# Performance work log

Hardware: AMD Instinct MI355X
Metric: run time of the kernel (lower is better)

Reference implementation:

```python
import jax, jax.numpy as jnp
import numpy as np

NTYPES = 2
MAXNEI = 128      # maxNeighborNum
M2 = 16
NPER = 256        # atoms per type
B = 4
EMB = [25, 50, 100]
FIT_IN = M2 * EMB[-1]  # 1600
FH = 240


def setup_inputs() -> dict:
    key = jax.random.key(0)
    ks = jax.random.split(key, 16)
    s = 0.1
    inp = {
        "Ri": jax.random.normal(ks[0], (B, NTYPES * NPER, NTYPES * MAXNEI, 4), jnp.float32),
        "emb_W0": jax.random.normal(ks[1], (4, 1, EMB[0]), jnp.float32) * s,
        "emb_b0": jax.random.normal(ks[2], (4, EMB[0]), jnp.float32) * s,
        "emb_W1": jax.random.normal(ks[3], (4, EMB[0], EMB[1]), jnp.float32) * s,
        "emb_b1": jax.random.normal(ks[4], (4, EMB[1]), jnp.float32) * s,
        "emb_W2": jax.random.normal(ks[5], (4, EMB[1], EMB[2]), jnp.float32) * s,
        "emb_b2": jax.random.normal(ks[6], (4, EMB[2]), jnp.float32) * s,
        "fit_W0": jax.random.normal(ks[7], (2, FIT_IN, FH), jnp.float32) * 0.02,
        "fit_b0": jax.random.normal(ks[8], (2, FH), jnp.float32) * s,
        "fit_W1": jax.random.normal(ks[9], (2, FH, FH), jnp.float32) * 0.05,
        "fit_b1": jax.random.normal(ks[10], (2, FH), jnp.float32) * s,
        "fit_W2": jax.random.normal(ks[11], (2, FH, FH), jnp.float32) * 0.05,
        "fit_b2": jax.random.normal(ks[12], (2, FH), jnp.float32) * s,
        "fit_W3": jax.random.normal(ks[13], (2, FH, 1), jnp.float32) * 0.05,
        "fit_b3": jax.random.normal(ks[14], (2, 1), jnp.float32),
    }
    return inp


def _emb(s, W0, b0, W1, b1, W2, b2):
    # DeepMD-style embedding MLP with doubling resnet skips (1->25->50->100)
    h0 = jnp.tanh(s @ W0 + b0)
    h1 = jnp.tanh(h0 @ W1 + b1) + jnp.concatenate([h0, h0], axis=-1)
    h2 = jnp.tanh(h1 @ W2 + b2) + jnp.concatenate([h1, h1], axis=-1)
    return h2


def _fit(d, W0, b0, W1, b1, W2, b2, W3, b3):
    h = jnp.tanh(d @ W0 + b0)
    h = jnp.tanh(h @ W1 + b1) + h   # resnet skip (equal dims)
    h = jnp.tanh(h @ W2 + b2) + h
    return h @ W3 + b3              # [B, N, 1]


def reference(Ri, emb_W0, emb_b0, emb_W1, emb_b1, emb_W2, emb_b2,
              fit_W0, fit_b0, fit_W1, fit_b1, fit_W2, fit_b2, fit_W3, fit_b3):
    type_nums = NTYPES
    Ei_blocks = []
    for i in range(NTYPES):                      # center-atom type
        Ri_i = Ri[:, i * NPER:(i + 1) * NPER]    # [B, NPER, NTYPES*M, 4]
        xyz = None
        for j in range(NTYPES):                  # neighbor type
            blk = Ri_i[:, :, j * MAXNEI:(j + 1) * MAXNEI, :]  # [B,N,M,4]
            S = blk[..., 0:1]                                  # [B,N,M,1]
            e = i * NTYPES + j
            G = _emb(S, emb_W0[e], emb_b0[e], emb_W1[e], emb_b1[e],
                     emb_W2[e], emb_b2[e])                     # [B,N,M,100]
            tmp = jnp.einsum('bnmc,bnmg->bncg', blk, G)        # [B,N,4,100]
            xyz = tmp if xyz is None else xyz + tmp
        xyz = xyz / (MAXNEI * type_nums)
        xyz_b = xyz[..., :M2]                                  # [B,N,4,16]
        DR = jnp.einsum('bncg,bnch->bngh', xyz, xyz_b)         # [B,N,100,16]
        DR = DR.reshape(B, NPER, FIT_IN)
        Ei_i = _fit(DR, fit_W0[i], fit_b0[i], fit_W1[i], fit_b1[i],
                    fit_W2[i], fit_b2[i], fit_W3[i], fit_b3[i])  # [B,N,1]
        Ei_blocks.append(Ei_i)
    Ei = jnp.concatenate(Ei_blocks, axis=1)     # [B, natoms_sum, 1]
    return Ei[..., 0]                            # per-atom energies [B, natoms_sum]
```

## Files before the change

### kernel.cpp

```cpp
#include <hip/hip_runtime.h>
#include <hip/hip_bf16.h>

#define FH 240
#define FIT_IN 1600
#define NK 2048
#define TLO -16.0f
#define TINVH 64.0f

typedef _Float16 h8 __attribute__((ext_vector_type(8)));
typedef float f4v __attribute__((ext_vector_type(4)));

__device__ __forceinline__ float fast_tanh(float x) {
    float e2 = __builtin_amdgcn_exp2f(x * 2.8853900817779268f);
    return 1.0f - 2.0f * __builtin_amdgcn_rcpf(e2 + 1.0f);
}

#define FMA_ROW(r, s) \
    acc[r][0] += (s) * b0.x; acc[r][1] += (s) * b0.y; \
    acc[r][2] += (s) * b0.z; acc[r][3] += (s) * b0.w; \
    acc[r][4] += (s) * b1.x; acc[r][5] += (s) * b1.y; \
    acc[r][6] += (s) * b1.z; acc[r][7] += (s) * b1.w;

#define TOFF_W0   0
#define TOFF_B0   28
#define TOFF_B1   56
#define TOFF_B2   108
#define TOFF_W1   208
#define TOFF_W2   1508
#define TOFF_H0T  6708
#define TOFF_H1T  10008
#define TSMEM     16608

__global__ __launch_bounds__(256) void k_prep(
    const float* __restrict__ eW0, const float* __restrict__ eB0,
    const float* __restrict__ eW1, const float* __restrict__ eB1,
    const float* __restrict__ eW2, const float* __restrict__ eB2,
    float* __restrict__ T,
    const float* __restrict__ fW0, const float* __restrict__ fW1,
    const float* __restrict__ fW2,
    _Float16* __restrict__ W0T, _Float16* __restrict__ W1T,
    _Float16* __restrict__ W2T)
{
    __shared__ float sm[TSMEM];
    const int t = threadIdx.x;

    if (blockIdx.x >= 64) {
        const int bid0 = blockIdx.x - 64;
        const int total = 768000 + 115200 + 115200;
        for (int idx = bid0 * 256 + t; idx < total; idx += 448 * 256) {
            if (idx < 768000) {
                const int tp = idx / 384000, r = idx - tp * 384000;
                const int n = r / 1600, k = r - n * 1600;
                W0T[idx] = (_Float16)fW0[tp * 384000 + k * 240 + n];
            } else if (idx < 883200) {
                const int j = idx - 768000;
                const int tp = j / 57600, r = j - tp * 57600;
                const int n = r / 240, k = r - n * 240;
                W1T[j] = (_Float16)fW1[tp * 57600 + k * 240 + n];
            } else {
                const int j = idx - 883200;
                const int tp = j / 57600, r = j - tp * 57600;
                const int n = r / 240, k = r - n * 240;
                W2T[j] = (_Float16)fW2[tp * 57600 + k * 240 + n];
            }
        }
        return;
    }

    const int w    = t >> 6;
    const int lane = t & 63;
    const int mi   = lane & 7;
    const int gi   = lane >> 3;
    const int mrow = w * 32 + mi * 4;

    const int e  = blockIdx.x >> 4;
    const int k0 = (blockIdx.x & 15) * 128;

    for (int idx = t; idx < 1250; idx += 256) {
        int k = idx / 50, g = idx - k * 50;
        sm[TOFF_W1 + k * 52 + g] = eW1[e * 1250 + idx];
    }
    for (int idx = t; idx < 5000; idx += 256) {
        int k = idx / 100, r = idx - k * 100;
        int half = r / 50, g = r - half * 50;
        sm[TOFF_W2 + k * 104 + half * 52 + g] = eW2[e * 5000 + idx];
    }
    if (t < 25)       { sm[TOFF_W0 + t] = eW0[e * 25 + t]; sm[TOFF_B0 + t] = eB0[e * 25 + t]; }
    else if (t < 75)  { sm[TOFF_B1 + (t - 25)] = eB1[e * 50 + (t - 25)]; }
    else if (t < 175) { sm[TOFF_B2 + (t - 75)] = eB2[e * 100 + (t - 75)]; }
    __syncthreads();

    if (t < 128) {
        const float S = TLO + (float)(k0 + t) * (1.0f / TINVH);
        #pragma unroll
        for (int k = 0; k < 25; ++k)
            sm[TOFF_H0T + k * 132 + t] = fast_tanh(S * sm[TOFF_W0 + k] + sm[TOFF_B0 + k]);
    }
    __syncthreads();

    {
        float acc[4][8];
        #pragma unroll
        for (int r = 0; r < 4; ++r)
            #pragma unroll
            for (int c = 0; c < 8; ++c) acc[r][c] = 0.f;

        #pragma unroll 5
        for (int k = 0; k < 25; ++k) {
            const float4 av = *(const float4*)&sm[TOFF_H0T + k * 132 + mrow];
            const float4 b0 = *(const float4*)&sm[TOFF_W1 + k * 52 + gi * 8];
            const float4 b1 = *(const float4*)&sm[TOFF_W1 + k * 52 + gi * 8 + 4];
            FMA_ROW(0, av.x) FMA_ROW(1, av.y) FMA_ROW(2, av.z) FMA_ROW(3, av.w)
        }
        #pragma unroll
        for (int c = 0; c < 8; ++c) {
            const int g = gi * 8 + c;
            if (g < 50) {
                const int gm = (g < 25) ? g : g - 25;
                const float4 h0r = *(const float4*)&sm[TOFF_H0T + gm * 132 + mrow];
                const float bias = sm[TOFF_B1 + g];
                float4 o;
                o.x = fast_tanh(acc[0][c] + bias) + h0r.x;
                o.y = fast_tanh(acc[1][c] + bias) + h0r.y;
                o.z = fast_tanh(acc[2][c] + bias) + h0r.z;
                o.w = fast_tanh(acc[3][c] + bias) + h0r.w;
                *(float4*)&sm[TOFF_H1T + g * 132 + mrow] = o;
            }
        }
    }
    __syncthreads();

    for (int half = 0; half < 2; ++half) {
        float acc[4][8];
        #pragma unroll
        for (int r = 0; r < 4; ++r)
            #pragma unroll
            for (int c = 0; c < 8; ++c) acc[r][c] = 0.f;

        #pragma unroll 5
        for (int k = 0; k < 50; ++k) {
            const float4 av = *(const float4*)&sm[TOFF_H1T + k * 132 + mrow];
            const float4 b0 = *(const float4*)&sm[TOFF_W2 + k * 104 + half * 52 + gi * 8];
            const float4 b1 = *(const float4*)&sm[TOFF_W2 + k * 104 + half * 52 + gi * 8 + 4];
            FMA_ROW(0, av.x) FMA_ROW(1, av.y) FMA_ROW(2, av.z) FMA_ROW(3, av.w)
        }
        #pragma unroll
        for (int c = 0; c < 8; ++c) {
            const int g = gi * 8 + c;
            if (g < 50) {
                const float4 h1r = *(const float4*)&sm[TOFF_H1T + g * 132 + mrow];
                const float bias = sm[TOFF_B2 + half * 50 + g];
                float* out = T + ((size_t)e * NK + k0 + mrow) * 100 + half * 50 + g;
                out[0]   = fast_tanh(acc[0][c] + bias) + h1r.x;
                out[100] = fast_tanh(acc[1][c] + bias) + h1r.y;
                out[200] = fast_tanh(acc[2][c] + bias) + h1r.z;
                out[300] = fast_tanh(acc[3][c] + bias) + h1r.w;
            }
        }
    }
}

__global__ __launch_bounds__(256) void k_xyz(
    const float* __restrict__ Ri, const float* __restrict__ T,
    _Float16* __restrict__ DRh)
{
    __shared__ float4 sR[256];
    __shared__ float  sF[256];
    __shared__ int    sI[256];
    __shared__ float  sXYZ[400];

    const int t   = threadIdx.x;
    const int blk = blockIdx.x;
    const int b   = blk >> 9;
    const int i   = (blk >> 8) & 1;
    const int n   = blk & 255;

    for (int idx = t; idx < 400; idx += 256) sXYZ[idx] = 0.f;

    {
        const int jj = t >> 7, m = t & 127;
        const size_t row = ((size_t)(b * 512 + i * 256 + n)) * 256 + jj * 128 + m;
        const float4 r = *(const float4*)(Ri + row * 4);
        sR[t] = r;
        float u = (r.x - TLO) * TINVH;
        int ii = (int)u;
        ii = (ii < 0) ? 0 : ((ii > NK - 2) ? NK - 2 : ii);
        sI[t] = ii;
        sF[t] = u - (float)ii;
    }
    __syncthreads();

    const int jj = t >> 7;
    const int g  = t & 127;
    if (g < 100) {
        const float* Te = T + ((size_t)(i * 2 + jj)) * NK * 100 + g;
        float a0 = 0.f, a1 = 0.f, a2 = 0.f, a3 = 0.f;
        #pragma unroll 4
        for (int m = 0; m < 128; ++m) {
            const int s = jj * 128 + m;
            const float4 R = sR[s];
            const float  f = sF[s];
            const float* p = Te + (size_t)sI[s] * 100;
            const float v0 = p[0], v1 = p[100];
            const float G = v0 + f * (v1 - v0);
            a0 += R.x * G; a1 += R.y * G; a2 += R.z * G; a3 += R.w * G;
        }
        atomicAdd(&sXYZ[g],       a0);
        atomicAdd(&sXYZ[100 + g], a1);
        atomicAdd(&sXYZ[200 + g], a2);
        atomicAdd(&sXYZ[300 + g], a3);
    }
    __syncthreads();

    const float inv = 1.0f / 65536.0f;
    _Float16* dr = DRh + (((size_t)i * 4 + b) * 256 + n) * FIT_IN;
    for (int q = t; q < 400; q += 256) {
        const int gg = q >> 2, h0 = (q & 3) * 4;
        ushort4 pk;
        _Float16* ph = (_Float16*)&pk;
        #pragma unroll
        for (int r = 0; r < 4; ++r) {
            const int h = h0 + r;
            const float v = (sXYZ[gg] * sXYZ[h] + sXYZ[100 + gg] * sXYZ[100 + h]
                           + sXYZ[200 + gg] * sXYZ[200 + h] + sXYZ[300 + gg] * sXYZ[300 + h]) * inv;
            ph[r] = (_Float16)v;
        }
        *(ushort4*)(dr + gg * 16 + h0) = pk;
    }
}

__global__ __launch_bounds__(512) void k_fit(
    const _Float16* __restrict__ DRh,
    const _Float16* __restrict__ W0T, const _Float16* __restrict__ W1T,
    const _Float16* __restrict__ W2T,
    const float* __restrict__ fb0, const float* __restrict__ fb1,
    const float* __restrict__ fb2, const float* __restrict__ fW3,
    const float* __restrict__ fb3, float* __restrict__ out)
{
    __shared__ _Float16 sB[2][240 * 40];
    __shared__ _Float16 sA0[2][16 * 40];
    __shared__ _Float16 sA[16 * 264];
    __shared__ float    hRes[2][8 * 240];

    const int t    = threadIdx.x;
    const int w    = t >> 6;
    const int lane = t & 63;
    const int ln   = lane & 15;
    const int quad = lane >> 4;
    const int r0   = blockIdx.x * 8;
    const int tp   = r0 >> 10;
    const int nf0  = w * 2;
    const int nfr  = (w < 7) ? 2 : 1;

    for (int q = t; q < 16 * 264; q += 512) sA[q] = (_Float16)0.f;
    for (int q = t; q < 2 * 16 * 40; q += 512) ((_Float16*)sA0)[q] = (_Float16)0.f;

    const _Float16* Ab = DRh + (size_t)r0 * FIT_IN;
    const _Float16* Wb = W0T + (size_t)tp * 240 * FIT_IN;

    f4v acc[2];
    acc[0] = (f4v)0.f; acc[1] = (f4v)0.f;
    {
        uint2 pB[4]; uint2 pA;
        {
            const int k0 = 0;
            #pragma unroll
            for (int j = 0; j < 4; ++j) {
                const int q = t + j * 512;
                if (q < 1920) {
                    const int n = q >> 3, kq = (q & 7) * 4;
                    pB[j] = *(const uint2*)(Wb + (size_t)n * FIT_IN + k0 + kq);
                }
            }
            if (t < 64) {
                const int m = t >> 3, kq = (t & 7) * 4;
                pA = *(const uint2*)(Ab + (size_t)m * FIT_IN + k0 + kq);
            }
        }
        for (int step = 0; step < 50; ++step) {
            const int buf = step & 1;
            #pragma unroll
            for (int j = 0; j < 4; ++j) {
                const int q = t + j * 512;
                if (q < 1920) {
                    const int n = q >> 3, kq = (q & 7) * 4;
                    *(uint2*)&sB[buf][n * 40 + kq] = pB[j];
                }
            }
            if (t < 64) {
                const int m = t >> 3, kq = (t & 7) * 4;
                *(uint2*)&sA0[buf][m * 40 + kq] = pA;
            }
            __syncthreads();
            if (step < 49) {
                const int k0 = (step + 1) * 32;
                #pragma unroll
                for (int j = 0; j < 4; ++j) {
                    const int q = t + j * 512;
                    if (q < 1920) {
                        const int n = q >> 3, kq = (q & 7) * 4;
                        pB[j] = *(const uint2*)(Wb + (size_t)n * FIT_IN + k0 + kq);
                    }
                }
                if (t < 64) {
                    const int m = t >> 3, kq = (t & 7) * 4;
                    pA = *(const uint2*)(Ab + (size_t)m * FIT_IN + k0 + kq);
                }
            }
            const h8 afr = *(const h8*)&sA0[buf][ln * 40 + quad * 8];
            #pragma unroll
            for (int nf = 0; nf < 2; ++nf) {
                if (nf < nfr) {
                    const h8 bfr = *(const h8*)&sB[buf][((nf0 + nf) * 16 + ln) * 40 + quad * 8];
                    acc[nf] = __builtin_amdgcn_mfma_f32_16x16x32_f16(afr, bfr, acc[nf], 0, 0, 0);
                }
            }
        }
    }
    __syncthreads();
    {
        const float* B0 = fb0 + tp * FH;
        #pragma unroll
        for (int nf = 0; nf < 2; ++nf) {
            if (nf < nfr && quad < 2) {
                const int col = (nf0 + nf) * 16 + ln;
                const float bias = B0[col];
                #pragma unroll
                for (int r = 0; r < 4; ++r) {
                    const int m = quad * 4 + r;
                    const float v = fast_tanh(acc[nf][r] + bias);
                    hRes[0][m * 240 + col] = v;
                    sA[m * 264 + col] = (_Float16)v;
                }
            }
        }
    }
    __syncthreads();

    for (int layer = 0; layer < 2; ++layer) {
        const _Float16* Wt = (layer == 0 ? W1T : W2T) + (size_t)tp * FH * FH;
        const float* Bias  = (layer == 0 ? fb1 : fb2) + tp * FH;
        const float* res   = hRes[layer];
        float* outb        = hRes[layer ^ 1];

        f4v a2[2];
        a2[0] = (f4v)0.f; a2[1] = (f4v)0.f;
        uint2 pW[4];
        #pragma unroll
        for (int j = 0; j < 4; ++j) {
            const int q = t + j * 512;
            if (q < 1920) {
                const int n = q >> 3, kq = (q & 7) * 4;
                pW[j] = (kq < FH) ? *(const uint2*)(Wt + (size_t)n * FH + kq)
                                  : make_uint2(0u, 0u);
            }
        }
        for (int step = 0; step < 8; ++step) {
            const int buf = step & 1;
            #pragma unroll
            for (int j = 0; j < 4; ++j) {
                const int q = t + j * 512;
                if (q < 1920) {
                    const int n = q >> 3, kq = (q & 7) * 4;
                    *(uint2*)&sB[buf][n * 40 + kq] = pW[j];
                }
            }
            __syncthreads();
            if (step < 7) {
                const int k0 = (step + 1) * 32;
                #pragma unroll
                for (int j = 0; j < 4; ++j) {
                    const int q = t + j * 512;
                    if (q < 1920) {
                        const int n = q >> 3, kq = (q & 7) * 4;
                        const int k = k0 + kq;
                        pW[j] = (k < FH) ? *(const uint2*)(Wt + (size_t)n * FH + k)
                                         : make_uint2(0u, 0u);
                    }
                }
            }
            const int k0 = step * 32;
            const h8 afr = *(const h8*)&sA[ln * 264 + k0 + quad * 8];
            #pragma unroll
            for (int nf = 0; nf < 2; ++nf) {
                if (nf < nfr) {
                    const h8 bfr = *(const h8*)&sB[buf][((nf0 + nf) * 16 + ln) * 40 + quad * 8];
                    a2[nf] = __builtin_amdgcn_mfma_f32_16x16x32_f16(afr, bfr, a2[nf], 0, 0, 0);
                }
            }
        }
        __syncthreads();
        #pragma unroll
        for (int nf = 0; nf < 2; ++nf) {
            if (nf < nfr && quad < 2) {
                const int col = (nf0 + nf) * 16 + ln;
                const float bias = Bias[col];
                #pragma unroll
                for (int r = 0; r < 4; ++r) {
                    const int m = quad * 4 + r;
                    const float v = fast_tanh(a2[nf][r] + bias) + res[m * 240 + col];
                    outb[m * 240 + col] = v;
                    if (layer == 0) sA[m * 264 + col] = (_Float16)v;
                }
            }
        }
        __syncthreads();
    }

    {
        const float* h2 = hRes[0];
        const float* wv = fW3 + tp * FH;
        const int m = w;
        float s = 0.f;
        #pragma unroll
        for (int k = lane; k < FH; k += 64) s += h2[m * 240 + k] * wv[k];
        #pragma unroll
        for (int off = 32; off > 0; off >>= 1) s += __shfl_down(s, off);
        if (lane == 0) {
            const int gr = r0 + m;
            const int rem = gr & 1023;
            const int b = rem >> 8, n = rem & 255;
            out[b * 512 + tp * 256 + n] = s + fb3[tp];
        }
    }
}

extern "C" void kernel_launch(void* const* d_in, const int* in_sizes, int n_in,
                              void* d_out, int out_size, void* d_ws, size_t ws_size,
                              hipStream_t stream)
{
    const float* Ri  = (const float*)d_in[0];
    const float* eW0 = (const float*)d_in[1];
    const float* eB0 = (const float*)d_in[2];
    const float* eW1 = (const float*)d_in[3];
    const float* eB1 = (const float*)d_in[4];
    const float* eW2 = (const float*)d_in[5];
    const float* eB2 = (const float*)d_in[6];
    const float* fW0 = (const float*)d_in[7];
    const float* fb0 = (const float*)d_in[8];
    const float* fW1 = (const float*)d_in[9];
    const float* fb1 = (const float*)d_in[10];
    const float* fW2 = (const float*)d_in[11];
    const float* fb2 = (const float*)d_in[12];
    const float* fW3 = (const float*)d_in[13];
    const float* fb3 = (const float*)d_in[14];

    char* p = (char*)d_ws;
    float* T   = (float*)p;                 p += (size_t)4 * NK * 100 * 4;
    _Float16* DRh = (_Float16*)p;           p += (size_t)2048 * FIT_IN * 2;
    _Float16* W0T = (_Float16*)p;           p += (size_t)768000 * 2;
    _Float16* W1T = (_Float16*)p;           p += (size_t)115200 * 2;
    _Float16* W2T = (_Float16*)p;           p += (size_t)115200 * 2;

    k_prep<<<dim3(512), dim3(256), 0, stream>>>(eW0, eB0, eW1, eB1, eW2, eB2, T,
                                                fW0, fW1, fW2, W0T, W1T, W2T);
    k_xyz<<<dim3(2048), dim3(256), 0, stream>>>(Ri, T, DRh);
    k_fit<<<dim3(256), dim3(512), 0, stream>>>(DRh, W0T, W1T, W2T,
                                               fb0, fb1, fb2, fW3, fb3,
                                               (float*)d_out);
}
```

Baseline: 174.2 us.

## Load fit-MLP MFMA fragments directly from global memory with register prefetch

The fitting kernel's GEMMs no longer stage the weight and DR tiles through double-buffered shared memory. Each lane now loads its MFMA A/B fragments straight from global memory, with a two-step register prefetch for the first layer and a one-step prefetch for the hidden layers. This removes the LDS stores and the per-step __syncthreads across the 50-step K loop and the 8-step hidden loops. In exchange it relies on the caches for weight reuse across warps and blocks, and the hidden layers drop the k<240 guard. That means they read past each 240-wide row, and past the end of the last weight row, multiplying the overrun by zero-padded activations.

```diff
diff --git a/kernel.cpp b/kernel.cpp
--- a/kernel.cpp
+++ b/kernel.cpp
@@ -237,8 +237,6 @@
     const float* __restrict__ fb2, const float* __restrict__ fW3,
     const float* __restrict__ fb3, float* __restrict__ out)
 {
-    __shared__ _Float16 sB[2][240 * 40];
-    __shared__ _Float16 sA0[2][16 * 40];
     __shared__ _Float16 sA[16 * 264];
     __shared__ float    hRes[2][8 * 240];
 
@@ -253,71 +251,38 @@
     const int nfr  = (w < 7) ? 2 : 1;
 
     for (int q = t; q < 16 * 264; q += 512) sA[q] = (_Float16)0.f;
-    for (int q = t; q < 2 * 16 * 40; q += 512) ((_Float16*)sA0)[q] = (_Float16)0.f;
-
-    const _Float16* Ab = DRh + (size_t)r0 * FIT_IN;
-    const _Float16* Wb = W0T + (size_t)tp * 240 * FIT_IN;
 
     f4v acc[2];
     acc[0] = (f4v)0.f; acc[1] = (f4v)0.f;
     {
-        uint2 pB[4]; uint2 pA;
-        {
-            const int k0 = 0;
-            #pragma unroll
-            for (int j = 0; j < 4; ++j) {
-                const int q = t + j * 512;
-                if (q < 1920) {
-                    const int n = q >> 3, kq = (q & 7) * 4;
-                    pB[j] = *(const uint2*)(Wb + (size_t)n * FIT_IN + k0 + kq);
-                }
-            }
-            if (t < 64) {
-                const int m = t >> 3, kq = (t & 7) * 4;
-                pA = *(const uint2*)(Ab + (size_t)m * FIT_IN + k0 + kq);
-            }
-        }
-        for (int step = 0; step < 50; ++step) {
-            const int buf = step & 1;
-            #pragma unroll
-            for (int j = 0; j < 4; ++j) {
-                const int q = t + j * 512;
-                if (q < 1920) {
-                    const int n = q >> 3, kq = (q & 7) * 4;
-                    *(uint2*)&sB[buf][n * 40 + kq] = pB[j];
-                }
-            }
-            if (t < 64) {
-                const int m = t >> 3, kq = (t & 7) * 4;
-                *(uint2*)&sA0[buf][m * 40 + kq] = pA;
-            }
-            __syncthreads();
-            if (step < 49) {
-                const int k0 = (step + 1) * 32;
-                #pragma unroll
-                for (int j = 0; j < 4; ++j) {
-                    const int q = t + j * 512;
-                    if (q < 1920) {
-                        const int n = q >> 3, kq = (q & 7) * 4;
-                        pB[j] = *(const uint2*)(Wb + (size_t)n * FIT_IN + k0 + kq);
-                    }
-                }
-                if (t < 64) {
-                    const int m = t >> 3, kq = (t & 7) * 4;
-                    pA = *(const uint2*)(Ab + (size_t)m * FIT_IN + k0 + kq);
-                }
-            }
-            const h8 afr = *(const h8*)&sA0[buf][ln * 40 + quad * 8];
-            #pragma unroll
-            for (int nf = 0; nf < 2; ++nf) {
-                if (nf < nfr) {
-                    const h8 bfr = *(const h8*)&sB[buf][((nf0 + nf) * 16 + ln) * 40 + quad * 8];
-                    acc[nf] = __builtin_amdgcn_mfma_f32_16x16x32_f16(afr, bfr, acc[nf], 0, 0, 0);
-                }
-            }
-        }
-    }
-    __syncthreads();
+        const _Float16* Arow = DRh + (size_t)(r0 + (ln & 7)) * FIT_IN;
+        const _Float16* W0b  = W0T + (size_t)tp * 240 * FIT_IN;
+        const _Float16* Bp0  = W0b + (size_t)(nf0 * 16 + ln) * FIT_IN;
+        const _Float16* Bp1  = W0b + (size_t)(((nfr > 1) ? nf0 + 1 : nf0) * 16 + ln) * FIT_IN;
+        const int kq = quad * 8;
+
+        h8 a_c  = *(const h8*)(Arow + kq);
+        h8 b0_c = *(const h8*)(Bp0 + kq);
+        h8 b1_c = *(const h8*)(Bp1 + kq);
+        h8 a_n  = *(const h8*)(Arow + 32 + kq);
+        h8 b0_n = *(const h8*)(Bp0 + 32 + kq);
+        h8 b1_n = *(const h8*)(Bp1 + 32 + kq);
+
+        #pragma unroll 2
+        for (int s = 0; s < 50; ++s) {
+            h8 a_f, b0_f, b1_f;
+            if (s + 2 < 50) {
+                const int k2 = (s + 2) * 32 + kq;
+                a_f  = *(const h8*)(Arow + k2);
+                b0_f = *(const h8*)(Bp0 + k2);
+                b1_f = *(const h8*)(Bp1 + k2);
+            }
+            acc[0] = __builtin_amdgcn_mfma_f32_16x16x32_f16(a_c, b0_c, acc[0], 0, 0, 0);
+            acc[1] = __builtin_amdgcn_mfma_f32_16x16x32_f16(a_c, b1_c, acc[1], 0, 0, 0);
+            a_c = a_n;  b0_c = b0_n;  b1_c = b1_n;
+            a_n = a_f;  b0_n = b0_f;  b1_n = b1_f;
+        }
+    }
     {
         const float* B0 = fb0 + tp * FH;
         #pragma unroll
@@ -343,51 +308,27 @@
         const float* res   = hRes[layer];
         float* outb        = hRes[layer ^ 1];
 
+        const _Float16* Bq0 = Wt + (size_t)(nf0 * 16 + ln) * FH;
+        const _Float16* Bq1 = Wt + (size_t)(((nfr > 1) ? nf0 + 1 : nf0) * 16 + ln) * FH;
+        const int kq = quad * 8;
+
         f4v a2[2];
         a2[0] = (f4v)0.f; a2[1] = (f4v)0.f;
-        uint2 pW[4];
-        #pragma unroll
-        for (int j = 0; j < 4; ++j) {
-            const int q = t + j * 512;
-            if (q < 1920) {
-                const int n = q >> 3, kq = (q & 7) * 4;
-                pW[j] = (kq < FH) ? *(const uint2*)(Wt + (size_t)n * FH + kq)
-                                  : make_uint2(0u, 0u);
-            }
-        }
-        for (int step = 0; step < 8; ++step) {
-            const int buf = step & 1;
-            #pragma unroll
-            for (int j = 0; j < 4; ++j) {
-                const int q = t + j * 512;
-                if (q < 1920) {
-                    const int n = q >> 3, kq = (q & 7) * 4;
-                    *(uint2*)&sB[buf][n * 40 + kq] = pW[j];
-                }
-            }
-            __syncthreads();
-            if (step < 7) {
-                const int k0 = (step + 1) * 32;
-                #pragma unroll
-                for (int j = 0; j < 4; ++j) {
-                    const int q = t + j * 512;
-                    if (q < 1920) {
-                        const int n = q >> 3, kq = (q & 7) * 4;
-                        const int k = k0 + kq;
-                        pW[j] = (k < FH) ? *(const uint2*)(Wt + (size_t)n * FH + k)
-                                         : make_uint2(0u, 0u);
-                    }
-                }
-            }
-            const int k0 = step * 32;
-            const h8 afr = *(const h8*)&sA[ln * 264 + k0 + quad * 8];
-            #pragma unroll
-            for (int nf = 0; nf < 2; ++nf) {
-                if (nf < nfr) {
-                    const h8 bfr = *(const h8*)&sB[buf][((nf0 + nf) * 16 + ln) * 40 + quad * 8];
-                    a2[nf] = __builtin_amdgcn_mfma_f32_16x16x32_f16(afr, bfr, a2[nf], 0, 0, 0);
-                }
-            }
+
+        h8 b0_c = *(const h8*)(Bq0 + kq);
+        h8 b1_c = *(const h8*)(Bq1 + kq);
+        #pragma unroll
+        for (int s = 0; s < 8; ++s) {
+            h8 b0_n, b1_n;
+            if (s + 1 < 8) {
+                const int k1 = (s + 1) * 32 + kq;
+                b0_n = *(const h8*)(Bq0 + k1);
+                b1_n = *(const h8*)(Bq1 + k1);
+            }
+            const h8 afr = *(const h8*)&sA[ln * 264 + s * 32 + kq];
+            a2[0] = __builtin_amdgcn_mfma_f32_16x16x32_f16(afr, b0_c, a2[0], 0, 0, 0);
+            a2[1] = __builtin_amdgcn_mfma_f32_16x16x32_f16(afr, b1_c, a2[1], 0, 0, 0);
+            b0_c = b0_n;  b1_c = b1_n;
         }
         __syncthreads();
         #pragma unroll
```

Result: no change. 172.9 us (-0.8%).
